# Performance work log

Measured on AMD Instinct MI355X. Metric: run time of the kernel, lower is better.

Reference implementation:

```python
import jax, jax.numpy as jnp
import numpy as np

B, M, T, L, K = 64, 16, 2048, 64, 32
N = T - L + 1  # 1985 sliding-window positions


def setup_inputs() -> dict:
    key = jax.random.key(0)
    k1, k2, k3 = jax.random.split(key, 3)
    x = jax.random.normal(k1, (B, M, T), dtype=jnp.float32)
    # shapelets initialized uniform(-1, 1) as in nn.init.uniform_
    shapelets = jax.random.uniform(k2, (K, L), dtype=jnp.float32, minval=-1.0, maxval=1.0)
    # penalty maps (learned; zeros at init, random here for a non-trivial weighting)
    penalty_maps = 0.1 * jax.random.normal(k3, (K, M, N), dtype=jnp.float32)
    return {"x": x, "shapelets": shapelets, "penalty_maps": penalty_maps}


def reference(x, shapelets, penalty_maps):
    # x: (B, M, T); shapelets: (K, L); penalty_maps: (K, M, N)
    Lw = shapelets.shape[1]
    n_pos = x.shape[2] - Lw + 1
    # sliding-window view: (B, M, N, L), equivalent to torch unfold(dim=2, size=L, step=1)
    idx = jnp.arange(n_pos)[:, None] + jnp.arange(Lw)[None, :]
    sub = x[:, :, idx]  # (B, M, N, L)

    def per_shapelet(args):
        shp, pmap = args  # (L,), (M, N)
        # raw squared L2 distance over window, per channel/position: (B, M, N)
        raw = jnp.sum((sub - shp[None, None, None, :]) ** 2, axis=3)
        pen = jax.nn.elu(-pmap) + 2.0  # (M, N)
        wd = jnp.sum(raw * pen[None], axis=1)  # sum over channels -> (B, N)
        return jnp.min(wd, axis=1)  # min over positions -> (B,)

    # sequential map over the K shapelets avoids a Kx blow-up of the (B,M,N,L) intermediate
    feats = jax.lax.map(per_shapelet, (shapelets, penalty_maps))  # (K, B)
    return feats.T  # (B, K)
```

## Files before the change

kernel.cpp:

```cpp
#include <hip/hip_runtime.h>
#include <hip/hip_bf16.h>

#define B_ 64
#define M_ 16
#define T_ 2048
#define L_ 64
#define K_ 32
#define N_ (T_ - L_ + 1)
#define NQP 512
#define TN 64
#define NTH 256
#define XROW 144
#define STSTR 72
#define SQSTR 64

typedef __attribute__((ext_vector_type(8))) short bf16x8;
typedef __attribute__((ext_vector_type(4))) float f32x4;

__device__ __forceinline__ unsigned short f2bf(float f) {
    __hip_bfloat16 h = __float2bfloat16(f);
    return __builtin_bit_cast(unsigned short, h);
}

__global__ void pen_init_kernel(const float* __restrict__ pmap,
                                const float* __restrict__ shp,
                                float* __restrict__ pen_t,
                                float* __restrict__ ss_ws,
                                unsigned* __restrict__ out) {
    const int gid = blockIdx.x * 256 + threadIdx.x;
    if (gid < B_ * K_) out[gid] = 0x7F800000u;
    if (gid < K_) {
        float s = 0.f;
        for (int l = 0; l < L_; ++l) { float v = shp[gid * L_ + l]; s = fmaf(v, v, s); }
        ss_ws[gid] = s;
    }
    if (gid < M_ * NQP * K_) {
        const int m  = gid >> 14;
        const int rem = gid & 16383;
        const int nq = rem >> 5;
        const int k  = rem & 31;
        const float* src = pmap + ((size_t)k * M_ + m) * N_;
        float4 r;
        float* pr = (float*)&r;
#pragma unroll
        for (int i = 0; i < 4; ++i) {
            int n = 4 * nq + i; if (n >= N_) n = N_ - 1;
            const float p = src[n];
            pr[i] = (p < 0.f) ? (2.f - p) : (__expf(-p) + 1.f);
        }
        *(float4*)(pen_t + (size_t)gid * 4) = r;
    }
}

__global__ __launch_bounds__(NTH, 2)
void shapelet_mfma_kernel(const float* __restrict__ x,
                          const float* __restrict__ shp,
                          const float* __restrict__ pen_t,
                          const float* __restrict__ ss_ws,
                          unsigned* __restrict__ out) {
    __shared__ __align__(16) unsigned short xbuf4[M_][4][XROW];
    __shared__ __align__(16) unsigned short st[K_][STSTR];
    __shared__ __align__(16) float sqw[M_][SQSTR];

    const int tid = threadIdx.x;
    const int n0 = blockIdx.x * TN;
    const int b  = blockIdx.y;
    const bool fast = (n0 + 128 <= T_);

    const float* xb = x + ((size_t)b * M_) * T_ + n0;
    for (int g = tid; g < M_ * 31; g += NTH) {
        const int m = g / 31, j4 = (g - m * 31) * 4;
        const float* src = xb + m * T_ + j4;
        float h[8];
        if (fast) {
            float4 v0 = *(const float4*)src;
            float4 v1 = *(const float4*)(src + 4);
            h[0] = v0.x; h[1] = v0.y; h[2] = v0.z; h[3] = v0.w;
            h[4] = v1.x; h[5] = v1.y; h[6] = v1.z; h[7] = v1.w;
        } else {
#pragma unroll
            for (int i = 0; i < 8; ++i)
                h[i] = (n0 + j4 + i < T_) ? src[i] : 0.f;
        }
        unsigned short hb[8];
#pragma unroll
        for (int i = 0; i < 8; ++i) hb[i] = f2bf(h[i]);
#pragma unroll
        for (int s = 0; s < 4; ++s) {
            ushort4 sv = { hb[s], hb[s + 1], hb[s + 2], hb[s + 3] };
            *(ushort4*)&xbuf4[m][s][j4] = sv;
        }
    }
    for (int i = tid; i < K_ * 16; i += NTH) {
        const int k = i >> 4, l4 = (i & 15) * 4;
        float4 v = *(const float4*)(shp + k * L_ + l4);
        ushort4 sv = { f2bf(v.x), f2bf(v.y), f2bf(v.z), f2bf(v.w) };
        *(ushort4*)&st[k][l4] = sv;
    }
    if (tid < M_ * 8) {
        const int m = tid >> 3, j0 = (tid & 7) * 8;
        const float* xr = x + ((size_t)b * M_ + m) * T_ + n0;
        float s = 0.f;
        if (fast) {
#pragma unroll
            for (int qd = 0; qd < 16; ++qd) {
                float4 v = *(const float4*)(xr + j0 + qd * 4);
                s = fmaf(v.x, v.x, s); s = fmaf(v.y, v.y, s);
                s = fmaf(v.z, v.z, s); s = fmaf(v.w, v.w, s);
            }
            sqw[m][j0] = s;
#pragma unroll
            for (int d = 1; d < 8; ++d) {
                float a = xr[j0 + d + L_ - 1], r = xr[j0 + d - 1];
                s += a * a - r * r;
                sqw[m][j0 + d] = s;
            }
        } else {
            for (int l = 0; l < L_; ++l) {
                float v = (n0 + j0 + l < T_) ? xr[j0 + l] : 0.f;
                s = fmaf(v, v, s);
            }
            sqw[m][j0] = s;
            for (int d = 1; d < 8; ++d) {
                float a = (n0 + j0 + d + L_ - 1 < T_) ? xr[j0 + d + L_ - 1] : 0.f;
                float r = (n0 + j0 + d - 1 < T_) ? xr[j0 + d - 1] : 0.f;
                s += a * a - r * r;
                sqw[m][j0 + d] = s;
            }
        }
    }
    __syncthreads();

    const int lane = tid & 63;
    const int w  = tid >> 6;
    const int rl = lane & 15;
    const int q  = lane >> 4;
    const int sp = rl & 3;
    const int e0 = 16 * w + 8 * q + (rl & ~3);
    const int eq = e0 >> 2;
    const int nrow = n0 + 16 * w + 4 * q;

    bf16x8 bfr[2][2];
#pragma unroll
    for (int t = 0; t < 2; ++t)
#pragma unroll
        for (int h = 0; h < 2; ++h)
            bfr[t][h] = *(const bf16x8*)&st[16 * t + rl][8 * q + 32 * h];

    const float ssk0 = ss_ws[rl], ssk1 = ss_ws[16 + rl];

    const int nq_l = (n0 >> 2) + 4 * w + q;
    const float* pt0 = pen_t + (((size_t)nq_l) * K_ + rl) * 4;

    f32x4 wd0 = (f32x4)0.f, wd1 = (f32x4)0.f;
    const f32x4 zero = (f32x4)0.f;

#pragma unroll 2
    for (int m = 0; m < M_; ++m) {
        float4 p0 = *(const float4*)(pt0 + (size_t)m * (NQP * K_ * 4));
        float4 p1 = *(const float4*)(pt0 + (size_t)m * (NQP * K_ * 4) + 64);

        const uint2* prow = (const uint2*)&xbuf4[m][sp][0];
        uint2 lo0 = prow[eq],     hi0 = prow[eq + 1];
        uint2 lo1 = prow[eq + 8], hi1 = prow[eq + 9];
        union { uint2 u2[2]; bf16x8 v; } fa0, fa1;
        fa0.u2[0] = lo0; fa0.u2[1] = hi0;
        fa1.u2[0] = lo1; fa1.u2[1] = hi1;

        f32x4 c0_ = __builtin_amdgcn_mfma_f32_16x16x32_bf16(fa0.v, bfr[0][0], zero, 0, 0, 0);
        c0_       = __builtin_amdgcn_mfma_f32_16x16x32_bf16(fa1.v, bfr[0][1], c0_, 0, 0, 0);
        f32x4 c1_ = __builtin_amdgcn_mfma_f32_16x16x32_bf16(fa0.v, bfr[1][0], zero, 0, 0, 0);
        c1_       = __builtin_amdgcn_mfma_f32_16x16x32_bf16(fa1.v, bfr[1][1], c1_, 0, 0, 0);

        f32x4 sq = *(const f32x4*)&sqw[m][16 * w + 4 * q];
        const float pe0[4] = { p0.x, p0.y, p0.z, p0.w };
        const float pe1[4] = { p1.x, p1.y, p1.z, p1.w };
#pragma unroll
        for (int r = 0; r < 4; ++r) {
            float t0v = fmaf(-2.f, c0_[r], sq[r] + ssk0);
            wd0[r] = fmaf(pe0[r], t0v, wd0[r]);
            float t1v = fmaf(-2.f, c1_[r], sq[r] + ssk1);
            wd1[r] = fmaf(pe1[r], t1v, wd1[r]);
        }
    }

#pragma unroll
    for (int t = 0; t < 2; ++t) {
        float lmin = __int_as_float(0x7F800000);
        const f32x4& wdv = t ? wd1 : wd0;
#pragma unroll
        for (int r = 0; r < 4; ++r) {
            if (nrow + r < N_) lmin = fminf(lmin, wdv[r]);
        }
        lmin = fminf(lmin, __shfl_xor(lmin, 16));
        lmin = fminf(lmin, __shfl_xor(lmin, 32));
        if (q == 0) {
            atomicMin(out + (size_t)b * K_ + 16 * t + rl,
                      __float_as_uint(fmaxf(lmin, 0.f)));
        }
    }
}

extern "C" void kernel_launch(void* const* d_in, const int* in_sizes, int n_in,
                              void* d_out, int out_size, void* d_ws, size_t ws_size,
                              hipStream_t stream) {
    const float* x    = (const float*)d_in[0];
    const float* shp  = (const float*)d_in[1];
    const float* pmap = (const float*)d_in[2];
    unsigned* out = (unsigned*)d_out;
    float* pen_t = (float*)d_ws;
    float* ss_ws = pen_t + (size_t)M_ * NQP * K_ * 4;

    const int work = M_ * NQP * K_;
    pen_init_kernel<<<dim3(work / 256), dim3(256), 0, stream>>>(
        pmap, shp, pen_t, ss_ws, out);

    dim3 grid((N_ + TN - 1) / TN, B_);
    shapelet_mfma_kernel<<<grid, dim3(NTH), 0, stream>>>(x, shp, pen_t, ss_ws, out);
}
```

Measured before the change: 101.3 us.

## Reuse penalty weights across four batches per block and store them as fp16

Each block now handles four batch entries in sequence. It loads its penalty weights (all 16 channels) and shapelet fragments into registers once and reuses them for every batch. The penalty table is stored in fp16 instead of fp32, which halves its workspace footprint and global read traffic. The trade-offs are a grid with a quarter as many blocks, higher register pressure that may reduce occupancy, extra barriers between batches, and a small loss of precision in the penalty weights.

```diff
diff --git a/kernel.cpp b/kernel.cpp
--- a/kernel.cpp
+++ b/kernel.cpp
@@ -1,4 +1,5 @@
 #include <hip/hip_runtime.h>
+#include <hip/hip_fp16.h>
 #include <hip/hip_bf16.h>
 
 #define B_ 64
@@ -9,6 +10,7 @@
 #define N_ (T_ - L_ + 1)
 #define NQP 512
 #define TN 64
+#define NBB 4
 #define NTH 256
 #define XROW 144
 #define STSTR 72
@@ -21,10 +23,13 @@
     __hip_bfloat16 h = __float2bfloat16(f);
     return __builtin_bit_cast(unsigned short, h);
 }
+__device__ __forceinline__ float h2f(unsigned short u) {
+    return __half2float(__builtin_bit_cast(__half, u));
+}
 
 __global__ void pen_init_kernel(const float* __restrict__ pmap,
                                 const float* __restrict__ shp,
-                                float* __restrict__ pen_t,
+                                unsigned short* __restrict__ pen_h,
                                 float* __restrict__ ss_ws,
                                 unsigned* __restrict__ out) {
     const int gid = blockIdx.x * 256 + threadIdx.x;
@@ -40,22 +45,23 @@
         const int nq = rem >> 5;
         const int k  = rem & 31;
         const float* src = pmap + ((size_t)k * M_ + m) * N_;
-        float4 r;
-        float* pr = (float*)&r;
+        ushort4 o;
+        unsigned short* po = (unsigned short*)&o;
 #pragma unroll
         for (int i = 0; i < 4; ++i) {
             int n = 4 * nq + i; if (n >= N_) n = N_ - 1;
             const float p = src[n];
-            pr[i] = (p < 0.f) ? (2.f - p) : (__expf(-p) + 1.f);
-        }
-        *(float4*)(pen_t + (size_t)gid * 4) = r;
+            const float pe = (p < 0.f) ? (2.f - p) : (__expf(-p) + 1.f);
+            po[i] = __builtin_bit_cast(unsigned short, __float2half(pe));
+        }
+        *(ushort4*)(pen_h + (size_t)gid * 4) = o;
     }
 }
 
 __global__ __launch_bounds__(NTH, 2)
 void shapelet_mfma_kernel(const float* __restrict__ x,
                           const float* __restrict__ shp,
-                          const float* __restrict__ pen_t,
+                          const unsigned short* __restrict__ pen_h,
                           const float* __restrict__ ss_ws,
                           unsigned* __restrict__ out) {
     __shared__ __align__(16) unsigned short xbuf4[M_][4][XROW];
@@ -64,72 +70,8 @@
 
     const int tid = threadIdx.x;
     const int n0 = blockIdx.x * TN;
-    const int b  = blockIdx.y;
+    const int b0 = blockIdx.y * NBB;
     const bool fast = (n0 + 128 <= T_);
-
-    const float* xb = x + ((size_t)b * M_) * T_ + n0;
-    for (int g = tid; g < M_ * 31; g += NTH) {
-        const int m = g / 31, j4 = (g - m * 31) * 4;
-        const float* src = xb + m * T_ + j4;
-        float h[8];
-        if (fast) {
-            float4 v0 = *(const float4*)src;
-            float4 v1 = *(const float4*)(src + 4);
-            h[0] = v0.x; h[1] = v0.y; h[2] = v0.z; h[3] = v0.w;
-            h[4] = v1.x; h[5] = v1.y; h[6] = v1.z; h[7] = v1.w;
-        } else {
-#pragma unroll
-            for (int i = 0; i < 8; ++i)
-                h[i] = (n0 + j4 + i < T_) ? src[i] : 0.f;
-        }
-        unsigned short hb[8];
-#pragma unroll
-        for (int i = 0; i < 8; ++i) hb[i] = f2bf(h[i]);
-#pragma unroll
-        for (int s = 0; s < 4; ++s) {
-            ushort4 sv = { hb[s], hb[s + 1], hb[s + 2], hb[s + 3] };
-            *(ushort4*)&xbuf4[m][s][j4] = sv;
-        }
-    }
-    for (int i = tid; i < K_ * 16; i += NTH) {
-        const int k = i >> 4, l4 = (i & 15) * 4;
-        float4 v = *(const float4*)(shp + k * L_ + l4);
-        ushort4 sv = { f2bf(v.x), f2bf(v.y), f2bf(v.z), f2bf(v.w) };
-        *(ushort4*)&st[k][l4] = sv;
-    }
-    if (tid < M_ * 8) {
-        const int m = tid >> 3, j0 = (tid & 7) * 8;
-        const float* xr = x + ((size_t)b * M_ + m) * T_ + n0;
-        float s = 0.f;
-        if (fast) {
-#pragma unroll
-            for (int qd = 0; qd < 16; ++qd) {
-                float4 v = *(const float4*)(xr + j0 + qd * 4);
-                s = fmaf(v.x, v.x, s); s = fmaf(v.y, v.y, s);
-                s = fmaf(v.z, v.z, s); s = fmaf(v.w, v.w, s);
-            }
-            sqw[m][j0] = s;
-#pragma unroll
-            for (int d = 1; d < 8; ++d) {
-                float a = xr[j0 + d + L_ - 1], r = xr[j0 + d - 1];
-                s += a * a - r * r;
-                sqw[m][j0 + d] = s;
-            }
-        } else {
-            for (int l = 0; l < L_; ++l) {
-                float v = (n0 + j0 + l < T_) ? xr[j0 + l] : 0.f;
-                s = fmaf(v, v, s);
-            }
-            sqw[m][j0] = s;
-            for (int d = 1; d < 8; ++d) {
-                float a = (n0 + j0 + d + L_ - 1 < T_) ? xr[j0 + d + L_ - 1] : 0.f;
-                float r = (n0 + j0 + d - 1 < T_) ? xr[j0 + d - 1] : 0.f;
-                s += a * a - r * r;
-                sqw[m][j0 + d] = s;
-            }
-        }
-    }
-    __syncthreads();
 
     const int lane = tid & 63;
     const int w  = tid >> 6;
@@ -140,64 +82,141 @@
     const int eq = e0 >> 2;
     const int nrow = n0 + 16 * w + 4 * q;
 
+    const int nq_l = (n0 >> 2) + 4 * w + q;
+    const unsigned short* pb = pen_h + (((size_t)nq_l) * K_ + rl) * 4;
+    ushort4 penr0[M_], penr1[M_];
+#pragma unroll
+    for (int m = 0; m < M_; ++m) {
+        penr0[m] = *(const ushort4*)(pb + (size_t)m * (NQP * K_ * 4));
+        penr1[m] = *(const ushort4*)(pb + (size_t)m * (NQP * K_ * 4) + 64);
+    }
+    const float ssk0 = ss_ws[rl], ssk1 = ss_ws[16 + rl];
+
+    for (int i = tid; i < K_ * 16; i += NTH) {
+        const int k = i >> 4, l4 = (i & 15) * 4;
+        float4 v = *(const float4*)(shp + k * L_ + l4);
+        ushort4 sv = { f2bf(v.x), f2bf(v.y), f2bf(v.z), f2bf(v.w) };
+        *(ushort4*)&st[k][l4] = sv;
+    }
+
     bf16x8 bfr[2][2];
-#pragma unroll
-    for (int t = 0; t < 2; ++t)
-#pragma unroll
-        for (int h = 0; h < 2; ++h)
-            bfr[t][h] = *(const bf16x8*)&st[16 * t + rl][8 * q + 32 * h];
-
-    const float ssk0 = ss_ws[rl], ssk1 = ss_ws[16 + rl];
-
-    const int nq_l = (n0 >> 2) + 4 * w + q;
-    const float* pt0 = pen_t + (((size_t)nq_l) * K_ + rl) * 4;
-
-    f32x4 wd0 = (f32x4)0.f, wd1 = (f32x4)0.f;
     const f32x4 zero = (f32x4)0.f;
 
-#pragma unroll 2
-    for (int m = 0; m < M_; ++m) {
-        float4 p0 = *(const float4*)(pt0 + (size_t)m * (NQP * K_ * 4));
-        float4 p1 = *(const float4*)(pt0 + (size_t)m * (NQP * K_ * 4) + 64);
-
-        const uint2* prow = (const uint2*)&xbuf4[m][sp][0];
-        uint2 lo0 = prow[eq],     hi0 = prow[eq + 1];
-        uint2 lo1 = prow[eq + 8], hi1 = prow[eq + 9];
-        union { uint2 u2[2]; bf16x8 v; } fa0, fa1;
-        fa0.u2[0] = lo0; fa0.u2[1] = hi0;
-        fa1.u2[0] = lo1; fa1.u2[1] = hi1;
-
-        f32x4 c0_ = __builtin_amdgcn_mfma_f32_16x16x32_bf16(fa0.v, bfr[0][0], zero, 0, 0, 0);
-        c0_       = __builtin_amdgcn_mfma_f32_16x16x32_bf16(fa1.v, bfr[0][1], c0_, 0, 0, 0);
-        f32x4 c1_ = __builtin_amdgcn_mfma_f32_16x16x32_bf16(fa0.v, bfr[1][0], zero, 0, 0, 0);
-        c1_       = __builtin_amdgcn_mfma_f32_16x16x32_bf16(fa1.v, bfr[1][1], c1_, 0, 0, 0);
-
-        f32x4 sq = *(const f32x4*)&sqw[m][16 * w + 4 * q];
-        const float pe0[4] = { p0.x, p0.y, p0.z, p0.w };
-        const float pe1[4] = { p1.x, p1.y, p1.z, p1.w };
-#pragma unroll
-        for (int r = 0; r < 4; ++r) {
-            float t0v = fmaf(-2.f, c0_[r], sq[r] + ssk0);
-            wd0[r] = fmaf(pe0[r], t0v, wd0[r]);
-            float t1v = fmaf(-2.f, c1_[r], sq[r] + ssk1);
-            wd1[r] = fmaf(pe1[r], t1v, wd1[r]);
-        }
-    }
-
-#pragma unroll
-    for (int t = 0; t < 2; ++t) {
-        float lmin = __int_as_float(0x7F800000);
-        const f32x4& wdv = t ? wd1 : wd0;
-#pragma unroll
-        for (int r = 0; r < 4; ++r) {
-            if (nrow + r < N_) lmin = fminf(lmin, wdv[r]);
-        }
-        lmin = fminf(lmin, __shfl_xor(lmin, 16));
-        lmin = fminf(lmin, __shfl_xor(lmin, 32));
-        if (q == 0) {
-            atomicMin(out + (size_t)b * K_ + 16 * t + rl,
-                      __float_as_uint(fmaxf(lmin, 0.f)));
-        }
+#pragma unroll 1
+    for (int bi = 0; bi < NBB; ++bi) {
+        const int b = b0 + bi;
+
+        const float* xb = x + ((size_t)b * M_) * T_ + n0;
+        for (int g = tid; g < M_ * 31; g += NTH) {
+            const int m = g / 31, j4 = (g - m * 31) * 4;
+            const float* src = xb + m * T_ + j4;
+            float h[8];
+            if (fast) {
+                float4 v0 = *(const float4*)src;
+                float4 v1 = *(const float4*)(src + 4);
+                h[0] = v0.x; h[1] = v0.y; h[2] = v0.z; h[3] = v0.w;
+                h[4] = v1.x; h[5] = v1.y; h[6] = v1.z; h[7] = v1.w;
+            } else {
+#pragma unroll
+                for (int i = 0; i < 8; ++i)
+                    h[i] = (n0 + j4 + i < T_) ? src[i] : 0.f;
+            }
+            unsigned short hb[8];
+#pragma unroll
+            for (int i = 0; i < 8; ++i) hb[i] = f2bf(h[i]);
+#pragma unroll
+            for (int s = 0; s < 4; ++s) {
+                ushort4 sv = { hb[s], hb[s + 1], hb[s + 2], hb[s + 3] };
+                *(ushort4*)&xbuf4[m][s][j4] = sv;
+            }
+        }
+        if (tid < M_ * 8) {
+            const int m = tid >> 3, j0 = (tid & 7) * 8;
+            const float* xr = x + ((size_t)b * M_ + m) * T_ + n0;
+            float s = 0.f;
+            if (fast) {
+#pragma unroll
+                for (int qd = 0; qd < 16; ++qd) {
+                    float4 v = *(const float4*)(xr + j0 + qd * 4);
+                    s = fmaf(v.x, v.x, s); s = fmaf(v.y, v.y, s);
+                    s = fmaf(v.z, v.z, s); s = fmaf(v.w, v.w, s);
+                }
+                sqw[m][j0] = s;
+#pragma unroll
+                for (int d = 1; d < 8; ++d) {
+                    float a = xr[j0 + d + L_ - 1], r = xr[j0 + d - 1];
+                    s += a * a - r * r;
+                    sqw[m][j0 + d] = s;
+                }
+            } else {
+                for (int l = 0; l < L_; ++l) {
+                    float v = (n0 + j0 + l < T_) ? xr[j0 + l] : 0.f;
+                    s = fmaf(v, v, s);
+                }
+                sqw[m][j0] = s;
+                for (int d = 1; d < 8; ++d) {
+                    float a = (n0 + j0 + d + L_ - 1 < T_) ? xr[j0 + d + L_ - 1] : 0.f;
+                    float r = (n0 + j0 + d - 1 < T_) ? xr[j0 + d - 1] : 0.f;
+                    s += a * a - r * r;
+                    sqw[m][j0 + d] = s;
+                }
+            }
+        }
+        __syncthreads();
+
+        if (bi == 0) {
+#pragma unroll
+            for (int t = 0; t < 2; ++t)
+#pragma unroll
+                for (int h = 0; h < 2; ++h)
+                    bfr[t][h] = *(const bf16x8*)&st[16 * t + rl][8 * q + 32 * h];
+        }
+
+        f32x4 wd0 = (f32x4)0.f, wd1 = (f32x4)0.f;
+#pragma unroll
+        for (int m = 0; m < M_; ++m) {
+            const uint2* prow = (const uint2*)&xbuf4[m][sp][0];
+            uint2 lo0 = prow[eq],     hi0 = prow[eq + 1];
+            uint2 lo1 = prow[eq + 8], hi1 = prow[eq + 9];
+            union { uint2 u2[2]; bf16x8 v; } fa0, fa1;
+            fa0.u2[0] = lo0; fa0.u2[1] = hi0;
+            fa1.u2[0] = lo1; fa1.u2[1] = hi1;
+
+            f32x4 c0_ = __builtin_amdgcn_mfma_f32_16x16x32_bf16(fa0.v, bfr[0][0], zero, 0, 0, 0);
+            c0_       = __builtin_amdgcn_mfma_f32_16x16x32_bf16(fa1.v, bfr[0][1], c0_, 0, 0, 0);
+            f32x4 c1_ = __builtin_amdgcn_mfma_f32_16x16x32_bf16(fa0.v, bfr[1][0], zero, 0, 0, 0);
+            c1_       = __builtin_amdgcn_mfma_f32_16x16x32_bf16(fa1.v, bfr[1][1], c1_, 0, 0, 0);
+
+            f32x4 sq = *(const f32x4*)&sqw[m][16 * w + 4 * q];
+            const float pe0[4] = { h2f(penr0[m].x), h2f(penr0[m].y),
+                                   h2f(penr0[m].z), h2f(penr0[m].w) };
+            const float pe1[4] = { h2f(penr1[m].x), h2f(penr1[m].y),
+                                   h2f(penr1[m].z), h2f(penr1[m].w) };
+#pragma unroll
+            for (int r = 0; r < 4; ++r) {
+                float t0v = fmaf(-2.f, c0_[r], sq[r] + ssk0);
+                wd0[r] = fmaf(pe0[r], t0v, wd0[r]);
+                float t1v = fmaf(-2.f, c1_[r], sq[r] + ssk1);
+                wd1[r] = fmaf(pe1[r], t1v, wd1[r]);
+            }
+        }
+
+#pragma unroll
+        for (int t = 0; t < 2; ++t) {
+            float lmin = __int_as_float(0x7F800000);
+            const f32x4& wdv = t ? wd1 : wd0;
+#pragma unroll
+            for (int r = 0; r < 4; ++r) {
+                if (nrow + r < N_) lmin = fminf(lmin, wdv[r]);
+            }
+            lmin = fminf(lmin, __shfl_xor(lmin, 16));
+            lmin = fminf(lmin, __shfl_xor(lmin, 32));
+            if (q == 0) {
+                atomicMin(out + (size_t)b * K_ + 16 * t + rl,
+                          __float_as_uint(fmaxf(lmin, 0.f)));
+            }
+        }
+        __syncthreads();
     }
 }
 
@@ -208,13 +227,13 @@
     const float* shp  = (const float*)d_in[1];
     const float* pmap = (const float*)d_in[2];
     unsigned* out = (unsigned*)d_out;
-    float* pen_t = (float*)d_ws;
-    float* ss_ws = pen_t + (size_t)M_ * NQP * K_ * 4;
+    unsigned short* pen_h = (unsigned short*)d_ws;
+    float* ss_ws = (float*)(pen_h + (size_t)M_ * NQP * K_ * 4);
 
     const int work = M_ * NQP * K_;
     pen_init_kernel<<<dim3(work / 256), dim3(256), 0, stream>>>(
-        pmap, shp, pen_t, ss_ws, out);
-
-    dim3 grid((N_ + TN - 1) / TN, B_);
-    shapelet_mfma_kernel<<<grid, dim3(NTH), 0, stream>>>(x, shp, pen_t, ss_ws, out);
-}
+        pmap, shp, pen_h, ss_ws, out);
+
+    dim3 grid((N_ + TN - 1) / TN, B_ / NBB);
+    shapelet_mfma_kernel<<<grid, dim3(NTH), 0, stream>>>(x, shp, pen_h, ss_ws, out);
+}
```

Result: slower. 132.7 us (+31.0%).

## Precompute bf16 x and window energies in a separate prep kernel

Applied to the files above, without the earlier changes.

Adds an xprep kernel that converts each x row to bf16 once and computes sliding-window squared sums into workspace. The main MFMA kernel then loads bf16 data per wave into wave-private shared buffers, builds the shifted copies with funnel shifts, and converts shapelet fragments straight into registers. Removing the block-wide __syncthreads and the fp32 loads lets it target three blocks per SM. The cost is an extra kernel launch plus a round trip of the bf16 and window-sum buffers through global memory.

```diff
diff --git a/kernel.cpp b/kernel.cpp
--- a/kernel.cpp
+++ b/kernel.cpp
@@ -8,11 +8,12 @@
 #define K_ 32
 #define N_ (T_ - L_ + 1)
 #define NQP 512
+#define XBS 2112
+#define SQS 2048
 #define TN 64
 #define NTH 256
-#define XROW 144
-#define STSTR 72
-#define SQSTR 64
+#define XRW 80
+#define SQWP 20
 
 typedef __attribute__((ext_vector_type(8))) short bf16x8;
 typedef __attribute__((ext_vector_type(4))) float f32x4;
@@ -20,6 +21,9 @@
 __device__ __forceinline__ unsigned short f2bf(float f) {
     __hip_bfloat16 h = __float2bfloat16(f);
     return __builtin_bit_cast(unsigned short, h);
+}
+__device__ __forceinline__ unsigned fun16(unsigned lo, unsigned hi) {
+    return (unsigned)(((((unsigned long long)hi) << 32) | lo) >> 16);
 }
 
 __global__ void pen_init_kernel(const float* __restrict__ pmap,
@@ -40,8 +44,7 @@
         const int nq = rem >> 5;
         const int k  = rem & 31;
         const float* src = pmap + ((size_t)k * M_ + m) * N_;
-        float4 r;
-        float* pr = (float*)&r;
+        float4 r; float* pr = (float*)&r;
 #pragma unroll
         for (int i = 0; i < 4; ++i) {
             int n = 4 * nq + i; if (n >= N_) n = N_ - 1;
@@ -52,102 +55,106 @@
     }
 }
 
-__global__ __launch_bounds__(NTH, 2)
-void shapelet_mfma_kernel(const float* __restrict__ x,
+__global__ __launch_bounds__(256)
+void xprep_kernel(const float* __restrict__ x,
+                  unsigned short* __restrict__ xbf,
+                  float* __restrict__ sqwin) {
+    __shared__ __align__(16) float xrow[T_ + 64];
+    const int r = blockIdx.x;
+    const int tid = threadIdx.x;
+    const float* src = x + (size_t)r * T_;
+#pragma unroll
+    for (int i = 0; i < 2; ++i) {
+        const int i4 = 4 * (tid + 256 * i);
+        float4 v = *(const float4*)(src + i4);
+        *(float4*)&xrow[i4] = v;
+        ushort4 sv = { f2bf(v.x), f2bf(v.y), f2bf(v.z), f2bf(v.w) };
+        *(ushort4*)(xbf + (size_t)r * XBS + i4) = sv;
+    }
+    if (tid < 16) *(float4*)&xrow[T_ + 4 * tid] = make_float4(0.f, 0.f, 0.f, 0.f);
+    if (tid < 16) {
+        ushort4 z = { 0, 0, 0, 0 };
+        *(ushort4*)(xbf + (size_t)r * XBS + T_ + 4 * tid) = z;
+    }
+    __syncthreads();
+    const int n0t = 8 * tid;
+    float s = 0.f;
+#pragma unroll
+    for (int qd = 0; qd < 16; ++qd) {
+        float4 v = *(const float4*)&xrow[n0t + 4 * qd];
+        s = fmaf(v.x, v.x, s); s = fmaf(v.y, v.y, s);
+        s = fmaf(v.z, v.z, s); s = fmaf(v.w, v.w, s);
+    }
+    float* dst = sqwin + (size_t)r * SQS + n0t;
+    dst[0] = s;
+#pragma unroll
+    for (int d = 1; d < 8; ++d) {
+        float a = xrow[n0t + d + L_ - 1], rm = xrow[n0t + d - 1];
+        s += a * a - rm * rm;
+        dst[d] = s;
+    }
+}
+
+__global__ __launch_bounds__(NTH, 3)
+void shapelet_mfma_kernel(const unsigned short* __restrict__ xbf,
+                          const float* __restrict__ sqwin,
                           const float* __restrict__ shp,
                           const float* __restrict__ pen_t,
                           const float* __restrict__ ss_ws,
                           unsigned* __restrict__ out) {
-    __shared__ __align__(16) unsigned short xbuf4[M_][4][XROW];
-    __shared__ __align__(16) unsigned short st[K_][STSTR];
-    __shared__ __align__(16) float sqw[M_][SQSTR];
+    __shared__ __align__(16) unsigned short xw[4][M_][4][XRW];
+    __shared__ __align__(16) float sqw[4][M_][SQWP];
 
     const int tid = threadIdx.x;
-    const int n0 = blockIdx.x * TN;
-    const int b  = blockIdx.y;
-    const bool fast = (n0 + 128 <= T_);
-
-    const float* xb = x + ((size_t)b * M_) * T_ + n0;
-    for (int g = tid; g < M_ * 31; g += NTH) {
-        const int m = g / 31, j4 = (g - m * 31) * 4;
-        const float* src = xb + m * T_ + j4;
-        float h[8];
-        if (fast) {
-            float4 v0 = *(const float4*)src;
-            float4 v1 = *(const float4*)(src + 4);
-            h[0] = v0.x; h[1] = v0.y; h[2] = v0.z; h[3] = v0.w;
-            h[4] = v1.x; h[5] = v1.y; h[6] = v1.z; h[7] = v1.w;
-        } else {
-#pragma unroll
-            for (int i = 0; i < 8; ++i)
-                h[i] = (n0 + j4 + i < T_) ? src[i] : 0.f;
-        }
-        unsigned short hb[8];
-#pragma unroll
-        for (int i = 0; i < 8; ++i) hb[i] = f2bf(h[i]);
-#pragma unroll
-        for (int s = 0; s < 4; ++s) {
-            ushort4 sv = { hb[s], hb[s + 1], hb[s + 2], hb[s + 3] };
-            *(ushort4*)&xbuf4[m][s][j4] = sv;
-        }
-    }
-    for (int i = tid; i < K_ * 16; i += NTH) {
-        const int k = i >> 4, l4 = (i & 15) * 4;
-        float4 v = *(const float4*)(shp + k * L_ + l4);
-        ushort4 sv = { f2bf(v.x), f2bf(v.y), f2bf(v.z), f2bf(v.w) };
-        *(ushort4*)&st[k][l4] = sv;
-    }
-    if (tid < M_ * 8) {
-        const int m = tid >> 3, j0 = (tid & 7) * 8;
-        const float* xr = x + ((size_t)b * M_ + m) * T_ + n0;
-        float s = 0.f;
-        if (fast) {
-#pragma unroll
-            for (int qd = 0; qd < 16; ++qd) {
-                float4 v = *(const float4*)(xr + j0 + qd * 4);
-                s = fmaf(v.x, v.x, s); s = fmaf(v.y, v.y, s);
-                s = fmaf(v.z, v.z, s); s = fmaf(v.w, v.w, s);
-            }
-            sqw[m][j0] = s;
-#pragma unroll
-            for (int d = 1; d < 8; ++d) {
-                float a = xr[j0 + d + L_ - 1], r = xr[j0 + d - 1];
-                s += a * a - r * r;
-                sqw[m][j0 + d] = s;
-            }
-        } else {
-            for (int l = 0; l < L_; ++l) {
-                float v = (n0 + j0 + l < T_) ? xr[j0 + l] : 0.f;
-                s = fmaf(v, v, s);
-            }
-            sqw[m][j0] = s;
-            for (int d = 1; d < 8; ++d) {
-                float a = (n0 + j0 + d + L_ - 1 < T_) ? xr[j0 + d + L_ - 1] : 0.f;
-                float r = (n0 + j0 + d - 1 < T_) ? xr[j0 + d - 1] : 0.f;
-                s += a * a - r * r;
-                sqw[m][j0 + d] = s;
-            }
-        }
-    }
-    __syncthreads();
-
     const int lane = tid & 63;
     const int w  = tid >> 6;
     const int rl = lane & 15;
     const int q  = lane >> 4;
+    const int n0 = blockIdx.x * TN;
+    const int b  = blockIdx.y;
+    const int nb = n0 + 16 * w;
+
+    for (int i = lane; i < M_ * 19; i += 64) {
+        const int m = i / 19, j4 = (i - m * 19) * 4;
+        const unsigned short* s8 = xbf + ((size_t)(b * M_ + m)) * XBS + nb + j4;
+        uint2 a = *(const uint2*)s8;
+        uint2 c = *(const uint2*)(s8 + 4);
+        const unsigned u0 = a.x, u1 = a.y, u2 = c.x, u3 = c.y;
+        const unsigned a01 = fun16(u0, u1);
+        const unsigned a12 = fun16(u1, u2);
+        const unsigned a23 = fun16(u2, u3);
+        uint2 p;
+        p.x = u0;  p.y = u1;  *(uint2*)&xw[w][m][0][j4] = p;
+        p.x = a01; p.y = a12; *(uint2*)&xw[w][m][1][j4] = p;
+        p.x = u1;  p.y = u2;  *(uint2*)&xw[w][m][2][j4] = p;
+        p.x = a12; p.y = a23; *(uint2*)&xw[w][m][3][j4] = p;
+    }
+    {
+        const int m = lane >> 2, n4 = (lane & 3) * 4;
+        float4 v = *(const float4*)(sqwin + ((size_t)(b * M_ + m)) * SQS + nb + n4);
+        *(float4*)&sqw[w][m][n4] = v;
+    }
+    bf16x8 bfr[2][2];
+#pragma unroll
+    for (int t = 0; t < 2; ++t)
+#pragma unroll
+        for (int h = 0; h < 2; ++h) {
+            const float* sp_ = shp + (16 * t + rl) * L_ + 8 * q + 32 * h;
+            float4 v0 = *(const float4*)sp_;
+            float4 v1 = *(const float4*)(sp_ + 4);
+            union { unsigned short us[8]; bf16x8 v; } cv;
+            cv.us[0] = f2bf(v0.x); cv.us[1] = f2bf(v0.y);
+            cv.us[2] = f2bf(v0.z); cv.us[3] = f2bf(v0.w);
+            cv.us[4] = f2bf(v1.x); cv.us[5] = f2bf(v1.y);
+            cv.us[6] = f2bf(v1.z); cv.us[7] = f2bf(v1.w);
+            bfr[t][h] = cv.v;
+        }
+
+    const float ssk0 = ss_ws[rl], ssk1 = ss_ws[16 + rl];
     const int sp = rl & 3;
-    const int e0 = 16 * w + 8 * q + (rl & ~3);
-    const int eq = e0 >> 2;
-    const int nrow = n0 + 16 * w + 4 * q;
-
-    bf16x8 bfr[2][2];
-#pragma unroll
-    for (int t = 0; t < 2; ++t)
-#pragma unroll
-        for (int h = 0; h < 2; ++h)
-            bfr[t][h] = *(const bf16x8*)&st[16 * t + rl][8 * q + 32 * h];
-
-    const float ssk0 = ss_ws[rl], ssk1 = ss_ws[16 + rl];
+    const int e0s = 8 * q + (rl & ~3);
+    const int eqi = e0s >> 2;
+    const int nrow = nb + 4 * q;
 
     const int nq_l = (n0 >> 2) + 4 * w + q;
     const float* pt0 = pen_t + (((size_t)nq_l) * K_ + rl) * 4;
@@ -160,9 +167,9 @@
         float4 p0 = *(const float4*)(pt0 + (size_t)m * (NQP * K_ * 4));
         float4 p1 = *(const float4*)(pt0 + (size_t)m * (NQP * K_ * 4) + 64);
 
-        const uint2* prow = (const uint2*)&xbuf4[m][sp][0];
-        uint2 lo0 = prow[eq],     hi0 = prow[eq + 1];
-        uint2 lo1 = prow[eq + 8], hi1 = prow[eq + 9];
+        const uint2* prow = (const uint2*)&xw[w][m][sp][0];
+        uint2 lo0 = prow[eqi],     hi0 = prow[eqi + 1];
+        uint2 lo1 = prow[eqi + 8], hi1 = prow[eqi + 9];
         union { uint2 u2[2]; bf16x8 v; } fa0, fa1;
         fa0.u2[0] = lo0; fa0.u2[1] = hi0;
         fa1.u2[0] = lo1; fa1.u2[1] = hi1;
@@ -172,7 +179,7 @@
         f32x4 c1_ = __builtin_amdgcn_mfma_f32_16x16x32_bf16(fa0.v, bfr[1][0], zero, 0, 0, 0);
         c1_       = __builtin_amdgcn_mfma_f32_16x16x32_bf16(fa1.v, bfr[1][1], c1_, 0, 0, 0);
 
-        f32x4 sq = *(const f32x4*)&sqw[m][16 * w + 4 * q];
+        f32x4 sq = *(const f32x4*)&sqw[w][m][4 * q];
         const float pe0[4] = { p0.x, p0.y, p0.z, p0.w };
         const float pe1[4] = { p1.x, p1.y, p1.z, p1.w };
 #pragma unroll
@@ -208,13 +215,17 @@
     const float* shp  = (const float*)d_in[1];
     const float* pmap = (const float*)d_in[2];
     unsigned* out = (unsigned*)d_out;
+
     float* pen_t = (float*)d_ws;
     float* ss_ws = pen_t + (size_t)M_ * NQP * K_ * 4;
-
-    const int work = M_ * NQP * K_;
-    pen_init_kernel<<<dim3(work / 256), dim3(256), 0, stream>>>(
+    unsigned short* xbf = (unsigned short*)(ss_ws + 64);
+    float* sqwin = (float*)(xbf + (size_t)B_ * M_ * XBS);
+
+    pen_init_kernel<<<dim3(M_ * NQP * K_ / 256), dim3(256), 0, stream>>>(
         pmap, shp, pen_t, ss_ws, out);
+    xprep_kernel<<<dim3(B_ * M_), dim3(256), 0, stream>>>(x, xbf, sqwin);
 
     dim3 grid((N_ + TN - 1) / TN, B_);
-    shapelet_mfma_kernel<<<grid, dim3(NTH), 0, stream>>>(x, shp, pen_t, ss_ws, out);
-}
+    shapelet_mfma_kernel<<<grid, dim3(NTH), 0, stream>>>(
+        xbf, sqwin, shp, pen_t, ss_ws, out);
+}
```

Result: no change. 102.1 us (+0.8%).
